# Kernel tuning notes

Hardware: AMD Instinct MI355X
Metric: run time of the kernel (lower is better)

Reference implementation:

```python
import jax, jax.numpy as jnp
import numpy as np

D_MODEL = 1024
N_HEADS = 16
D_HEAD = D_MODEL // N_HEADS
D_FF = 2048
B, S = 4, 1024
EPS = 1e-6


def layernorm(x, gamma, beta):
    mu = jnp.mean(x, axis=-1, keepdims=True)
    var = jnp.mean(jnp.square(x - mu), axis=-1, keepdims=True)
    return (x - mu) * jax.lax.rsqrt(var + EPS) * gamma + beta


def setup_inputs() -> dict:
    key = jax.random.key(0)
    ks = jax.random.split(key, 12)
    s = 0.02
    return {
        "x": jax.random.normal(ks[0], (B, S, D_MODEL), jnp.float32),
        "mask": jnp.ones((B, 1, 1, S), jnp.int32),
        "Wq": jax.random.normal(ks[1], (D_MODEL, D_MODEL), jnp.float32) * s,
        "Wk": jax.random.normal(ks[2], (D_MODEL, D_MODEL), jnp.float32) * s,
        "Wv": jax.random.normal(ks[3], (D_MODEL, D_MODEL), jnp.float32) * s,
        "Wo": jax.random.normal(ks[4], (D_MODEL, D_MODEL), jnp.float32) * s,
        "bo": jnp.zeros((D_MODEL,), jnp.float32),
        "ln1_g": jnp.ones((D_MODEL,), jnp.float32),
        "ln1_b": jnp.zeros((D_MODEL,), jnp.float32),
        "W1": jax.random.normal(ks[5], (D_MODEL, D_FF), jnp.float32) * s,
        "b1": jnp.zeros((D_FF,), jnp.float32),
        "W2": jax.random.normal(ks[6], (D_FF, D_MODEL), jnp.float32) * s,
        "b2": jnp.zeros((D_MODEL,), jnp.float32),
        "ln2_g": jnp.ones((D_MODEL,), jnp.float32),
        "ln2_b": jnp.zeros((D_MODEL,), jnp.float32),
    }


def reference(x, mask, Wq, Wk, Wv, Wo, bo, ln1_g, ln1_b, W1, b1, W2, b2, ln2_g, ln2_b):
    b, s, _ = x.shape
    # --- multi-head attention ---
    q_proj = x @ Wq                      # [B,S,D]
    k_proj = x @ Wk
    v_proj = x @ Wv
    q = q_proj.reshape(b, s, N_HEADS, D_HEAD)
    k = k_proj.reshape(b, s, N_HEADS, D_HEAD)
    v = v_proj.reshape(b, s, N_HEADS, D_HEAD)
    attn = jnp.einsum('bqhd,bkhd->bhqk', q, k)           # [B,H,S,S]
    attn = jnp.where(mask == 0, -jnp.inf, attn)
    attn = jax.nn.softmax(attn / jnp.sqrt(jnp.float32(D_MODEL)), axis=-1)
    out = jnp.einsum('bhqk,bkhd->bqhd', attn, v).reshape(b, s, D_MODEL)
    # source applies ReLU after the output projection, dropout=eval identity
    out = jax.nn.relu(out @ Wo + bo) + q_proj            # residual = projected queries
    out = layernorm(out, ln1_g, ln1_b)
    # --- FFN (source applies activation AFTER linear2) ---
    ff = jax.nn.relu((out @ W1 + b1) @ W2 + b2) + out
    return layernorm(ff, ln2_g, ln2_b)
```

## Files before the change

### kernel.cpp

```cpp
#include <hip/hip_runtime.h>
#include <hip/hip_bf16.h>

#define D_MODEL 1024
#define N_HEADS 16
#define D_HEAD  64
#define D_FF    2048
#define BATCH   4
#define SEQ     1024
#define ROWS    (BATCH*SEQ)

typedef __bf16  bf16x8 __attribute__((ext_vector_type(8)));
typedef float   f32x4  __attribute__((ext_vector_type(4)));
typedef unsigned int u32x4 __attribute__((ext_vector_type(4)));
typedef unsigned int u32x2 __attribute__((ext_vector_type(2)));
typedef unsigned short u16;
typedef unsigned int u32;

__device__ inline u16 f2bf(float x){ __hip_bfloat16 b = __float2bfloat16(x); return *(u16*)&b; }

__device__ inline void load_lds16(const u16* gsrc, u16* ldst){
  __builtin_amdgcn_global_load_lds((const __attribute__((address_space(1))) void*)gsrc,
                                   (__attribute__((address_space(3))) void*)ldst, 16, 0, 0);
}

__global__ __launch_bounds__(256)
void cast_bf16_kernel(const float* __restrict__ src, __hip_bfloat16* __restrict__ dst, int n){
  int i = (blockIdx.x*blockDim.x + threadIdx.x)*4;
  if (i + 3 < n){
    float4 v = *(const float4*)(src + i);
    dst[i+0] = __float2bfloat16(v.x);
    dst[i+1] = __float2bfloat16(v.y);
    dst[i+2] = __float2bfloat16(v.z);
    dst[i+3] = __float2bfloat16(v.w);
  }
}

__global__ __launch_bounds__(256)
void transpose_cast_kernel(const float* __restrict__ src, __hip_bfloat16* __restrict__ dst,
                           int R, int C){
  __shared__ float tile[32][33];
  int c0 = blockIdx.x*32, r0 = blockIdx.y*32;
  int tx = threadIdx.x & 31, ty = threadIdx.x >> 5;
  #pragma unroll
  for (int i=0;i<32;i+=8)
    tile[ty+i][tx] = src[(size_t)(r0+ty+i)*C + (c0+tx)];
  __syncthreads();
  #pragma unroll
  for (int i=0;i<32;i+=8)
    dst[(size_t)(c0+ty+i)*R + (r0+tx)] = __float2bfloat16(tile[tx][ty+i]);
}

__global__ __launch_bounds__(256)
void transpose4_kernel(const float* __restrict__ s0, const float* __restrict__ s1,
                       const float* __restrict__ s2, const float* __restrict__ s3,
                       __hip_bfloat16* __restrict__ dst){
  __shared__ float tile[32][33];
  const float* src = (blockIdx.z==0)?s0:(blockIdx.z==1)?s1:(blockIdx.z==2)?s2:s3;
  __hip_bfloat16* d = dst + (size_t)blockIdx.z*1024*1024;
  int c0 = blockIdx.x*32, r0 = blockIdx.y*32;
  int tx = threadIdx.x & 31, ty = threadIdx.x >> 5;
  #pragma unroll
  for (int i=0;i<32;i+=8)
    tile[ty+i][tx] = src[(size_t)(r0+ty+i)*1024 + (c0+tx)];
  __syncthreads();
  #pragma unroll
  for (int i=0;i<32;i+=8)
    d[(size_t)(c0+ty+i)*1024 + (r0+tx)] = __float2bfloat16(tile[tx][ty+i]);
}

template<int MODE, int BN>
__global__ __launch_bounds__(256, 2)
void gemm_bt_kernel(const u16* __restrict__ A, const u16* __restrict__ BT,
                    const float* __restrict__ bias, const float* __restrict__ res,
                    float* __restrict__ Cf, __hip_bfloat16* __restrict__ Cb,
                    int M, int N, int K, float cscale){
  __shared__ u16 As[2][128*32];
  __shared__ u16 Bs[2][BN*32];
  const int m0 = blockIdx.y*128, n0 = blockIdx.x*BN;
  const int t = threadIdx.x;
  const int wid = t>>6, lane = t&63;
  const int wm = wid>>1, wn = wid&1;
  const int lr = lane&15, lk = (lane>>4)*8;
  const int srow = t>>2, sseg = (t&3)*8;
  const int wbase = wid*512;

  constexpr int NJ = BN/32;
  f32x4 acc[4][NJ] = {};
  const int NK = K/32;

  #pragma unroll
  for (int c=0;c<2;++c)
    load_lds16(A + (size_t)(m0 + c*64 + srow)*K + sseg, &As[0][c*2048 + wbase]);
  #pragma unroll
  for (int c=0;c<BN/64;++c)
    load_lds16(BT + (size_t)(n0 + c*64 + srow)*K + sseg, &Bs[0][c*2048 + wbase]);
  __syncthreads();

  for (int kt=0; kt<NK; ++kt){
    const int cur = kt&1;
    if (kt+1 < NK){
      const int kn = (kt+1)*32;
      #pragma unroll
      for (int c=0;c<2;++c)
        load_lds16(A + (size_t)(m0 + c*64 + srow)*K + kn + sseg, &As[cur^1][c*2048 + wbase]);
      #pragma unroll
      for (int c=0;c<BN/64;++c)
        load_lds16(BT + (size_t)(n0 + c*64 + srow)*K + kn + sseg, &Bs[cur^1][c*2048 + wbase]);
    }
    bf16x8 af[4], bfr[NJ];
    #pragma unroll
    for (int f=0; f<4; ++f)
      af[f]  = *(const bf16x8*)&As[cur][(wm*64 + f*16 + lr)*32 + lk];
    #pragma unroll
    for (int j=0; j<NJ; ++j)
      bfr[j] = *(const bf16x8*)&Bs[cur][(wn*(BN/2) + j*16 + lr)*32 + lk];
    #pragma unroll
    for (int i=0;i<4;++i)
      #pragma unroll
      for (int j=0;j<NJ;++j)
        acc[i][j] = __builtin_amdgcn_mfma_f32_16x16x32_bf16(af[i], bfr[j], acc[i][j], 0,0,0);
    __syncthreads();
  }

  const int r_in = (lane>>4)*4;
  #pragma unroll
  for (int i=0;i<4;++i){
    #pragma unroll
    for (int j=0;j<NJ;++j){
      int col = n0 + wn*(BN/2) + j*16 + lr;
      float bv = bias ? bias[col] : 0.f;
      #pragma unroll
      for (int e=0;e<4;++e){
        int row = m0 + wm*64 + i*16 + r_in + e;
        float v = acc[i][j][e] + bv;
        if (MODE == 0){
          Cf[(size_t)row*N + col] = v;
        } else if (MODE == 1){
          Cb[(size_t)row*N + col] = __float2bfloat16(v);
        } else if (MODE == 6){
          Cf[(size_t)row*N + col] = fmaxf(v,0.f) + res[(size_t)row*N + col];
        } else {
          int b = row>>10, s = row&1023;
          int which = col>>10, c = col&1023, h = c>>6, d = c&63;
          size_t hm = (((size_t)b*16 + h)*1024 + s)*64 + d;
          if (which == 0){
            Cf[(size_t)row*1024 + c] = v;
            Cb[hm] = __float2bfloat16(v * cscale);
          } else if (which == 1){
            Cb[4194304u + hm] = __float2bfloat16(v);
          } else {
            Cb[8388608u + (((size_t)b*16 + h)*64 + d)*1024 + s] = __float2bfloat16(v);
          }
        }
      }
    }
  }
}

__global__ __launch_bounds__(512)
void attn_mfma_kernel(const u16* __restrict__ qb, const u16* __restrict__ kb,
                      const u16* __restrict__ vt, const int* __restrict__ mask,
                      __hip_bfloat16* __restrict__ out){
  __shared__ u16 Ks[2][64*72];
  __shared__ u16 Vs[2][64*72];
  __shared__ u16 Pl[8][16*72];
  const int t = threadIdx.x;
  const int wid = t>>6, lane = t&63;
  const int lr = lane&15, lg = lane>>4, lk = lg*8;
  const int bid = blockIdx.x;
  const int xcd = bid & 7, slot = bid >> 3;
  const int bh = xcd*8 + (slot>>3);
  const int qx = slot & 7;
  const int b = bh>>4, h = bh&15;
  const int q0 = qx*128 + wid*16;
  const u16* qbase = qb + (size_t)bh*1024*64;
  const u16* kbase = kb + (size_t)bh*1024*64;
  const u16* vbase = vt + (size_t)bh*64*1024;
  const int* mrow = mask + b*SEQ;

  bf16x8 aq[2];
  aq[0] = *(const bf16x8*)(qbase + (size_t)(q0+lr)*64 + lk);
  aq[1] = *(const bf16x8*)(qbase + (size_t)(q0+lr)*64 + 32 + lk);

  f32x4 osum[4] = {};
  float m1 = -1e30f, l1 = 0.f;

  const int sr = t>>3, sg = (t&7)*8;
  {
    u32x4 kr = *(const u32x4*)(kbase + (size_t)sr*64 + sg);
    u32x4 vr = *(const u32x4*)(vbase + (size_t)sr*1024 + sg);
    *(u32x4*)&Ks[0][sr*72+sg] = kr;
    *(u32x4*)&Vs[0][sr*72+sg] = vr;
  }
  __syncthreads();

  for (int kt=0; kt<SEQ/64; ++kt){
    const int k0 = kt*64;
    const int cur = kt&1;
    u32x4 kr, vr;
    const bool more = (kt+1 < SEQ/64);
    if (more){
      kr = *(const u32x4*)(kbase + (size_t)(k0+64+sr)*64 + sg);
      vr = *(const u32x4*)(vbase + (size_t)sr*1024 + (k0+64) + sg);
    }

    unsigned long long bm = __ballot(mrow[k0 + lane] != 0);

    f32x4 sacc[4] = {};
    __builtin_amdgcn_s_setprio(1);
    #pragma unroll
    for (int k4=0;k4<4;++k4){
      #pragma unroll
      for (int dg=0;dg<2;++dg){
        bf16x8 kf = *(const bf16x8*)&Ks[cur][(k4*16+lr)*72 + dg*32 + lk];
        sacc[k4] = __builtin_amdgcn_mfma_f32_16x16x32_bf16(kf, aq[dg], sacc[k4],0,0,0);
      }
    }
    __builtin_amdgcn_s_setprio(0);
    if (bm != ~0ull){
      #pragma unroll
      for (int k4=0;k4<4;++k4)
        #pragma unroll
        for (int e=0;e<4;++e)
          if (!((bm >> (k4*16 + lg*4 + e)) & 1)) sacc[k4][e] = -1e30f;
    }

    float tm = -1e30f;
    #pragma unroll
    for (int k4=0;k4<4;++k4)
      #pragma unroll
      for (int e=0;e<4;++e) tm = fmaxf(tm, sacc[k4][e]);
    tm = fmaxf(tm, __shfl_xor(tm,16));
    tm = fmaxf(tm, __shfl_xor(tm,32));

    float mn = m1, c = 1.f;
    bool need = !__all(tm <= m1 + 8.f);
    if (need){
      mn = fmaxf(m1, tm);
      c  = exp2f(m1 - mn);
      m1 = mn;
    }
    float ps = 0.f;
    #pragma unroll
    for (int k4=0;k4<4;++k4)
      #pragma unroll
      for (int e=0;e<4;++e){ float p = exp2f(sacc[k4][e]-mn); sacc[k4][e]=p; ps+=p; }
    ps += __shfl_xor(ps,16);
    ps += __shfl_xor(ps,32);
    l1 = l1*c + ps;

    if (need){
      float ce[4];
      #pragma unroll
      for (int e=0;e<4;++e) ce[e] = __shfl(c, lg*4+e);
      #pragma unroll
      for (int dt=0;dt<4;++dt)
        #pragma unroll
        for (int e=0;e<4;++e) osum[dt][e] *= ce[e];
    }

    #pragma unroll
    for (int k4=0;k4<4;++k4){
      u32 lo = (u32)f2bf(sacc[k4][0]) | ((u32)f2bf(sacc[k4][1])<<16);
      u32 hi = (u32)f2bf(sacc[k4][2]) | ((u32)f2bf(sacc[k4][3])<<16);
      u32x2 pk; pk[0]=lo; pk[1]=hi;
      *(u32x2*)&Pl[wid][lr*72 + k4*16 + lg*4] = pk;
    }
    __builtin_amdgcn_s_setprio(1);
    #pragma unroll
    for (int dt=0;dt<4;++dt){
      #pragma unroll
      for (int kg=0;kg<2;++kg){
        bf16x8 pa = *(const bf16x8*)&Pl[wid][lr*72 + kg*32 + lk];
        bf16x8 vf = *(const bf16x8*)&Vs[cur][(dt*16+lr)*72 + kg*32 + lk];
        osum[dt] = __builtin_amdgcn_mfma_f32_16x16x32_bf16(pa, vf, osum[dt],0,0,0);
      }
    }
    __builtin_amdgcn_s_setprio(0);

    if (more){
      *(u32x4*)&Ks[cur^1][sr*72+sg] = kr;
      *(u32x4*)&Vs[cur^1][sr*72+sg] = vr;
    }
    __syncthreads();
  }
  float li[4];
  #pragma unroll
  for (int e=0;e<4;++e) li[e] = 1.f / __shfl(l1, lg*4+e);
  #pragma unroll
  for (int dt=0;dt<4;++dt){
    int d = dt*16 + lr;
    #pragma unroll
    for (int e=0;e<4;++e){
      int q = q0 + lg*4 + e;
      out[((size_t)b*1024 + q)*1024 + h*64 + d] = __float2bfloat16(osum[dt][e] * li[e]);
    }
  }
}

__global__ __launch_bounds__(256)
void ln_kernel(const float* __restrict__ a, const float* __restrict__ g,
               const float* __restrict__ be, float* __restrict__ outf,
               __hip_bfloat16* __restrict__ outb){
  int row = blockIdx.x, t = threadIdx.x;
  size_t rb = (size_t)row*D_MODEL;
  float4 av = *(const float4*)(a + rb + t*4);
  float v0 = av.x, v1 = av.y, v2 = av.z, v3 = av.w;
  float sum = v0+v1+v2+v3;
  float ss  = v0*v0+v1*v1+v2*v2+v3*v3;
  #pragma unroll
  for (int off=32; off; off>>=1){ sum += __shfl_xor(sum,off); ss += __shfl_xor(ss,off); }
  __shared__ float red[8];
  int wid = t>>6, lane = t&63;
  if (lane==0){ red[wid]=sum; red[4+wid]=ss; }
  __syncthreads();
  sum = red[0]+red[1]+red[2]+red[3];
  ss  = red[4]+red[5]+red[6]+red[7];
  float mu  = sum*(1.f/1024.f);
  float var = ss*(1.f/1024.f) - mu*mu;
  float rstd = rsqrtf(var + 1e-6f);
  float4 gv = *(const float4*)(g  + t*4);
  float4 bv = *(const float4*)(be + t*4);
  float y0=(v0-mu)*rstd*gv.x+bv.x;
  float y1=(v1-mu)*rstd*gv.y+bv.y;
  float y2=(v2-mu)*rstd*gv.z+bv.z;
  float y3=(v3-mu)*rstd*gv.w+bv.w;
  *(float4*)(outf+rb+t*4) = make_float4(y0,y1,y2,y3);
  if (outb){
    outb[rb+t*4+0]=__float2bfloat16(y0);
    outb[rb+t*4+1]=__float2bfloat16(y1);
    outb[rb+t*4+2]=__float2bfloat16(y2);
    outb[rb+t*4+3]=__float2bfloat16(y3);
  }
}

extern "C" void kernel_launch(void* const* d_in, const int* in_sizes, int n_in,
                              void* d_out, int out_size, void* d_ws, size_t ws_size,
                              hipStream_t stream){
  const float* x    = (const float*)d_in[0];
  const int*   mask = (const int*)  d_in[1];
  const float* Wq   = (const float*)d_in[2];
  const float* Wk   = (const float*)d_in[3];
  const float* Wv   = (const float*)d_in[4];
  const float* Wo   = (const float*)d_in[5];
  const float* bo   = (const float*)d_in[6];
  const float* ln1g = (const float*)d_in[7];
  const float* ln1b = (const float*)d_in[8];
  const float* W1   = (const float*)d_in[9];
  const float* b1   = (const float*)d_in[10];
  const float* W2   = (const float*)d_in[11];
  const float* b2   = (const float*)d_in[12];
  const float* ln2g = (const float*)d_in[13];
  const float* ln2b = (const float*)d_in[14];

  char* ws = (char*)d_ws;
  const size_t MB = 1024*1024;
  __hip_bfloat16* WqT  = (__hip_bfloat16*)(ws + 0);
  __hip_bfloat16* WoT  = (__hip_bfloat16*)(ws + 6*MB);
  __hip_bfloat16* W1T  = (__hip_bfloat16*)(ws + 8*MB);
  __hip_bfloat16* W2T  = (__hip_bfloat16*)(ws + 12*MB);
  __hip_bfloat16* xb   = (__hip_bfloat16*)(ws + 16*MB);
  float* q_proj        = (float*)(ws + 24*MB);
  __hip_bfloat16* qb   = (__hip_bfloat16*)(ws + 40*MB);
  __hip_bfloat16* attn_o = (__hip_bfloat16*)(ws + 64*MB);
  float* t1f           = (float*)(ws + 40*MB);
  float* h1f           = (float*)(ws + 56*MB);
  __hip_bfloat16* h1b  = (__hip_bfloat16*)(ws + 16*MB);
  __hip_bfloat16* ff1b = (__hip_bfloat16*)(ws + 24*MB);
  float* t2f           = (float*)(ws + 40*MB);

  const float qscale = 0.03125f * 1.44269504f;

  cast_bf16_kernel<<<ROWS*D_MODEL/4/256, 256, 0, stream>>>(x, xb, ROWS*D_MODEL);
  transpose4_kernel<<<dim3(32,32,4), 256, 0, stream>>>(Wq, Wk, Wv, Wo, WqT);
  transpose_cast_kernel<<<dim3(64,32), 256, 0, stream>>>(W1, W1T, 1024, 2048);
  transpose_cast_kernel<<<dim3(32,64), 256, 0, stream>>>(W2, W2T, 2048, 1024);

  gemm_bt_kernel<5,128><<<dim3(24,32), 256, 0, stream>>>((const u16*)xb, (const u16*)WqT, nullptr,
                                                     nullptr, q_proj, qb, ROWS, 3072, 1024, qscale);

  attn_mfma_kernel<<<512, 512, 0, stream>>>(
      (const u16*)qb, (const u16*)(qb + 4194304u), (const u16*)(qb + 8388608u), mask, attn_o);

  gemm_bt_kernel<6,64><<<dim3(16,32), 256, 0, stream>>>((const u16*)attn_o, (const u16*)WoT, bo,
                                                    q_proj, t1f, nullptr, ROWS, 1024, 1024, 1.f);

  ln_kernel<<<ROWS, 256, 0, stream>>>(t1f, ln1g, ln1b, h1f, h1b);

  gemm_bt_kernel<1,128><<<dim3(16,32), 256, 0, stream>>>((const u16*)h1b, (const u16*)W1T, b1,
                                                     nullptr, nullptr, ff1b, ROWS, 2048, 1024, 1.f);

  gemm_bt_kernel<6,64><<<dim3(16,32), 256, 0, stream>>>((const u16*)ff1b, (const u16*)W2T, b2,
                                                    h1f, t2f, nullptr, ROWS, 1024, 2048, 1.f);

  ln_kernel<<<ROWS, 256, 0, stream>>>(t2f, ln2g, ln2b, (float*)d_out, nullptr);
}
```

Measured before the change: 205.8 us.

## Triple-buffer GEMM loads and use bf16 residuals instead of fp32 intermediates

The GEMM kernel moves from a two-stage to a three-stage LDS pipeline. It uses explicit vmcnt waits and raw barriers so loads for two tiles ahead stay in flight. The fp32 q_proj and h1f buffers are removed: the output-projection residual is rebuilt from the scaled bf16 Q tensor, and the FFN residual comes from the bf16 layernorm output. This cuts global memory traffic and stores, at the cost of bf16 rounding in the residual paths and more LDS per block.

```diff
diff --git a/kernel.cpp b/kernel.cpp
--- a/kernel.cpp
+++ b/kernel.cpp
@@ -71,11 +71,11 @@
 template<int MODE, int BN>
 __global__ __launch_bounds__(256, 2)
 void gemm_bt_kernel(const u16* __restrict__ A, const u16* __restrict__ BT,
-                    const float* __restrict__ bias, const float* __restrict__ res,
+                    const float* __restrict__ bias, const __hip_bfloat16* __restrict__ resb,
                     float* __restrict__ Cf, __hip_bfloat16* __restrict__ Cb,
                     int M, int N, int K, float cscale){
-  __shared__ u16 As[2][128*32];
-  __shared__ u16 Bs[2][BN*32];
+  __shared__ u16 As[3][128*32];
+  __shared__ u16 Bs[3][BN*32];
   const int m0 = blockIdx.y*128, n0 = blockIdx.x*BN;
   const int t = threadIdx.x;
   const int wid = t>>6, lane = t&63;
@@ -88,25 +88,25 @@
   f32x4 acc[4][NJ] = {};
   const int NK = K/32;
 
-  #pragma unroll
-  for (int c=0;c<2;++c)
-    load_lds16(A + (size_t)(m0 + c*64 + srow)*K + sseg, &As[0][c*2048 + wbase]);
-  #pragma unroll
-  for (int c=0;c<BN/64;++c)
-    load_lds16(BT + (size_t)(n0 + c*64 + srow)*K + sseg, &Bs[0][c*2048 + wbase]);
-  __syncthreads();
+  auto STAGE = [&](int s, int bi){
+    const int kn = s*32;
+    #pragma unroll
+    for (int c=0;c<2;++c)
+      load_lds16(A + (size_t)(m0 + c*64 + srow)*K + kn + sseg, &As[bi][c*2048 + wbase]);
+    #pragma unroll
+    for (int c=0;c<BN/64;++c)
+      load_lds16(BT + (size_t)(n0 + c*64 + srow)*K + kn + sseg, &Bs[bi][c*2048 + wbase]);
+  };
+
+  STAGE(0,0);
+  STAGE(1,1);
+  if constexpr (BN==128) asm volatile("s_waitcnt vmcnt(4)" ::: "memory");
+  else                   asm volatile("s_waitcnt vmcnt(3)" ::: "memory");
+  __builtin_amdgcn_s_barrier();
 
   for (int kt=0; kt<NK; ++kt){
-    const int cur = kt&1;
-    if (kt+1 < NK){
-      const int kn = (kt+1)*32;
-      #pragma unroll
-      for (int c=0;c<2;++c)
-        load_lds16(A + (size_t)(m0 + c*64 + srow)*K + kn + sseg, &As[cur^1][c*2048 + wbase]);
-      #pragma unroll
-      for (int c=0;c<BN/64;++c)
-        load_lds16(BT + (size_t)(n0 + c*64 + srow)*K + kn + sseg, &Bs[cur^1][c*2048 + wbase]);
-    }
+    const int cur = kt%3;
+    if (kt+2 < NK) STAGE(kt+2, (kt+2)%3);
     bf16x8 af[4], bfr[NJ];
     #pragma unroll
     for (int f=0; f<4; ++f)
@@ -119,7 +119,14 @@
       #pragma unroll
       for (int j=0;j<NJ;++j)
         acc[i][j] = __builtin_amdgcn_mfma_f32_16x16x32_bf16(af[i], bfr[j], acc[i][j], 0,0,0);
-    __syncthreads();
+    if (kt+2 < NK){
+      if constexpr (BN==128) asm volatile("s_waitcnt vmcnt(4)" ::: "memory");
+      else                   asm volatile("s_waitcnt vmcnt(3)" ::: "memory");
+      __builtin_amdgcn_s_barrier();
+    } else if (kt+1 < NK){
+      asm volatile("s_waitcnt vmcnt(0)" ::: "memory");
+      __builtin_amdgcn_s_barrier();
+    }
   }
 
   const int r_in = (lane>>4)*4;
@@ -133,18 +140,20 @@
       for (int e=0;e<4;++e){
         int row = m0 + wm*64 + i*16 + r_in + e;
         float v = acc[i][j][e] + bv;
-        if (MODE == 0){
-          Cf[(size_t)row*N + col] = v;
-        } else if (MODE == 1){
+        if (MODE == 1){
           Cb[(size_t)row*N + col] = __float2bfloat16(v);
         } else if (MODE == 6){
-          Cf[(size_t)row*N + col] = fmaxf(v,0.f) + res[(size_t)row*N + col];
+          Cf[(size_t)row*N + col] = fmaxf(v,0.f)
+              + __bfloat162float(resb[(size_t)row*N + col]);
+        } else if (MODE == 7){
+          int b = row>>10, s = row&1023, h = col>>6, d = col&63;
+          size_t hm = (((size_t)b*16 + h)*1024 + s)*64 + d;
+          Cf[(size_t)row*N + col] = fmaxf(v,0.f) + __bfloat162float(resb[hm])*cscale;
         } else {
           int b = row>>10, s = row&1023;
           int which = col>>10, c = col&1023, h = c>>6, d = c&63;
           size_t hm = (((size_t)b*16 + h)*1024 + s)*64 + d;
           if (which == 0){
-            Cf[(size_t)row*1024 + c] = v;
             Cb[hm] = __float2bfloat16(v * cscale);
           } else if (which == 1){
             Cb[4194304u + hm] = __float2bfloat16(v);
@@ -325,7 +334,7 @@
   float y1=(v1-mu)*rstd*gv.y+bv.y;
   float y2=(v2-mu)*rstd*gv.z+bv.z;
   float y3=(v3-mu)*rstd*gv.w+bv.w;
-  *(float4*)(outf+rb+t*4) = make_float4(y0,y1,y2,y3);
+  if (outf) *(float4*)(outf+rb+t*4) = make_float4(y0,y1,y2,y3);
   if (outb){
     outb[rb+t*4+0]=__float2bfloat16(y0);
     outb[rb+t*4+1]=__float2bfloat16(y1);
@@ -360,16 +369,15 @@
   __hip_bfloat16* W1T  = (__hip_bfloat16*)(ws + 8*MB);
   __hip_bfloat16* W2T  = (__hip_bfloat16*)(ws + 12*MB);
   __hip_bfloat16* xb   = (__hip_bfloat16*)(ws + 16*MB);
-  float* q_proj        = (float*)(ws + 24*MB);
+  __hip_bfloat16* h1b  = (__hip_bfloat16*)(ws + 16*MB);
+  float* t1f           = (float*)(ws + 24*MB);
+  __hip_bfloat16* ff1b = (__hip_bfloat16*)(ws + 24*MB);
   __hip_bfloat16* qb   = (__hip_bfloat16*)(ws + 40*MB);
+  float* t2f           = (float*)(ws + 40*MB);
   __hip_bfloat16* attn_o = (__hip_bfloat16*)(ws + 64*MB);
-  float* t1f           = (float*)(ws + 40*MB);
-  float* h1f           = (float*)(ws + 56*MB);
-  __hip_bfloat16* h1b  = (__hip_bfloat16*)(ws + 16*MB);
-  __hip_bfloat16* ff1b = (__hip_bfloat16*)(ws + 24*MB);
-  float* t2f           = (float*)(ws + 40*MB);
 
   const float qscale = 0.03125f * 1.44269504f;
+  const float qunscale = 1.0f / qscale;
 
   cast_bf16_kernel<<<ROWS*D_MODEL/4/256, 256, 0, stream>>>(x, xb, ROWS*D_MODEL);
   transpose4_kernel<<<dim3(32,32,4), 256, 0, stream>>>(Wq, Wk, Wv, Wo, WqT);
@@ -377,21 +385,21 @@
   transpose_cast_kernel<<<dim3(32,64), 256, 0, stream>>>(W2, W2T, 2048, 1024);
 
   gemm_bt_kernel<5,128><<<dim3(24,32), 256, 0, stream>>>((const u16*)xb, (const u16*)WqT, nullptr,
-                                                     nullptr, q_proj, qb, ROWS, 3072, 1024, qscale);
+                                                     nullptr, nullptr, qb, ROWS, 3072, 1024, qscale);
 
   attn_mfma_kernel<<<512, 512, 0, stream>>>(
       (const u16*)qb, (const u16*)(qb + 4194304u), (const u16*)(qb + 8388608u), mask, attn_o);
 
-  gemm_bt_kernel<6,64><<<dim3(16,32), 256, 0, stream>>>((const u16*)attn_o, (const u16*)WoT, bo,
-                                                    q_proj, t1f, nullptr, ROWS, 1024, 1024, 1.f);
-
-  ln_kernel<<<ROWS, 256, 0, stream>>>(t1f, ln1g, ln1b, h1f, h1b);
+  gemm_bt_kernel<7,64><<<dim3(16,32), 256, 0, stream>>>((const u16*)attn_o, (const u16*)WoT, bo,
+                                                    qb, t1f, nullptr, ROWS, 1024, 1024, qunscale);
+
+  ln_kernel<<<ROWS, 256, 0, stream>>>(t1f, ln1g, ln1b, nullptr, h1b);
 
   gemm_bt_kernel<1,128><<<dim3(16,32), 256, 0, stream>>>((const u16*)h1b, (const u16*)W1T, b1,
                                                      nullptr, nullptr, ff1b, ROWS, 2048, 1024, 1.f);
 
   gemm_bt_kernel<6,64><<<dim3(16,32), 256, 0, stream>>>((const u16*)ff1b, (const u16*)W2T, b2,
-                                                    h1f, t2f, nullptr, ROWS, 1024, 2048, 1.f);
+                                                    h1b, t2f, nullptr, ROWS, 1024, 2048, 1.f);
 
   ln_kernel<<<ROWS, 256, 0, stream>>>(t2f, ln2g, ln2b, (float*)d_out, nullptr);
 }
```

Measured after the change: 209.7 us. About the same (+1.9%).
